# Performance work log

Hardware: AMD Instinct MI355X
Metric: run time of the kernel (lower is better)

## Reference

```python
import jax, jax.numpy as jnp
import numpy as np

DIM = 256; N_HEADS = 8; HEAD_DIM = DIM // N_HEADS
RELU_DIM = 1024; LN_DIM = 512; N_LN = 2; EMB_DIM = 256
VOCAB = 32000; N_CLASSES = 16; B = 8; SEQ = 256
N_ITERS = 12   # fixed-point iterations of the DEQ solve (ITFn2)
EPS = 1e-5     # torch LayerNorm default eps


def sinusoidal_pos_emb(T, d):
    pos = np.arange(T)[:, None].astype(np.float32)
    i = np.arange(d // 2)[None, :].astype(np.float32)
    ang = pos / np.power(10000.0, 2.0 * i / d)
    pe = np.zeros((T, d), np.float32)
    pe[:, 0::2] = np.sin(ang)
    pe[:, 1::2] = np.cos(ang)
    return jnp.asarray(pe)


def setup_inputs() -> dict:
    key = jax.random.key(0)
    ks = jax.random.split(key, 8)
    x = jax.random.randint(ks[0], (B, SEQ), 0, VOCAB)
    seq_lens = jax.random.randint(ks[1], (B,), 1, SEQ + 1)
    emb = jax.random.normal(ks[2], (VOCAB + 1, EMB_DIM), jnp.float32) * EMB_DIM ** -0.5
    emb = emb.at[VOCAB].set(0.0)  # padding_idx row
    cls_token = jax.random.normal(ks[3], (1, 1, EMB_DIM), jnp.float32) * EMB_DIM ** -0.5
    # scaled down vs kaiming so the fixed-point map is contractive (module enforces this via project())
    A = jax.random.normal(ks[4], (RELU_DIM + LN_DIM, RELU_DIM + LN_DIM + DIM + EMB_DIM), jnp.float32) * 0.01
    b = jnp.zeros((RELU_DIM + LN_DIM,), jnp.float32)
    A_qkv = jax.random.normal(ks[5], (3 * DIM, LN_DIM), jnp.float32) * (2.0 / LN_DIM) ** 0.5
    W_cls = jax.random.normal(ks[6], (N_CLASSES, RELU_DIM + LN_DIM + DIM), jnp.float32) * (RELU_DIM + LN_DIM + DIM) ** -0.5
    b_cls = jnp.zeros((N_CLASSES,), jnp.float32)
    return {"x": x, "seq_lens": seq_lens, "emb": emb, "cls_token": cls_token,
            "A": A, "A_qkv": A_qkv, "b": b, "W_cls": W_cls, "b_cls": b_cls}


def reference(x, seq_lens, emb, cls_token, A, A_qkv, b, W_cls, b_cls):
    Bsz, T = x.shape
    Tp = T + 1
    # input injection: embed + sinusoidal pos, then prepend cls token
    u = emb[x] + sinusoidal_pos_emb(T, EMB_DIM)[None]
    u = jnp.concatenate([jnp.broadcast_to(cls_token, (Bsz, 1, EMB_DIM)), u], axis=1)  # (B, T+1, E)
    pos = jnp.arange(Tp)
    src_mask = (seq_lens[:, None] + 1) <= pos[None]  # (B, T+1), True = padded key
    # A_qkv rows ordered (n_heads, 3, head_dim) per scale_by_S rearrange
    Wqkv = A_qkv.reshape(N_HEADS, 3, HEAD_DIM, LN_DIM)
    scale = 1.0 / jnp.sqrt(jnp.asarray(HEAD_DIM, u.dtype))
    neg = jnp.asarray(-1e9, u.dtype)

    def step(z, _):
        # pre-activations for relu + layernorm blocks
        pre = jnp.einsum('btj,ij->bti', jnp.concatenate([z, u], axis=-1), A) + b
        z_r = jax.nn.relu(pre[..., :RELU_DIM])
        zl = pre[..., RELU_DIM:].reshape(Bsz, Tp, N_LN, LN_DIM // N_LN)
        mu = zl.mean(-1, keepdims=True)
        var = zl.var(-1, keepdims=True)
        z_l = ((zl - mu) * jax.lax.rsqrt(var + EPS)).reshape(Bsz, Tp, LN_DIM)
        # multi-head attention driven by the layernorm block
        qkv = jnp.einsum('btj,hmdj->bthmd', z_l, Wqkv)  # (B, T+1, H, 3, hd)
        q, k, v = qkv[..., 0, :], qkv[..., 1, :], qkv[..., 2, :]
        scores = jnp.einsum('bqhd,bkhd->bhqk', q, k) * scale
        scores = jnp.where(src_mask[:, None, None, :], neg, scores)
        attn = jax.nn.softmax(scores, axis=-1)
        z_a = jnp.einsum('bhqk,bkhd->bqhd', attn, v).reshape(Bsz, Tp, DIM)
        return jnp.concatenate([z_r, z_l, z_a], axis=-1), None

    z0 = jnp.zeros((Bsz, Tp, RELU_DIM + LN_DIM + DIM), u.dtype)
    z, _ = jax.lax.scan(step, z0, None, length=N_ITERS)
    # classify from the equilibrium cls-token state
    return z[:, 0] @ W_cls.T + b_cls
```

## Files before the change

### kernel.cpp

```cpp
#include <hip/hip_runtime.h>
#include <hip/hip_bf16.h>
#include <math.h>

#define TP 257
#define ROWS 2056
#define XDIM 2048
#define ZDIM 1792
#define PREDIM 1536
#define QKVDIM 768
#define EMBD 256

using f32x4  = __attribute__((ext_vector_type(4))) float;
using bf16x8 = __attribute__((ext_vector_type(8))) short;

__device__ __forceinline__ ushort f2bf(float f) {
    uint32_t u = __float_as_uint(f);
    return (ushort)((u + 0x7fffu + ((u >> 16) & 1u)) >> 16);
}
__device__ __forceinline__ float bf2f(ushort u) {
    return __uint_as_float(((uint32_t)u) << 16);
}

#define GLD16(g, l) __builtin_amdgcn_global_load_lds( \
    (const __attribute__((address_space(1))) void*)(g), \
    (__attribute__((address_space(3))) void*)(l), 16, 0, 0)

__global__ __launch_bounds__(256) void f2bf_kernel(
    const float* __restrict__ in, ushort* __restrict__ out, int n)
{
    int i = blockIdx.x * 256 + threadIdx.x;
    if (i < n) out[i] = f2bf(in[i]);
}

__global__ __launch_bounds__(256) void build_u_kernel(
    const int* __restrict__ x, const float* __restrict__ emb,
    const float* __restrict__ cls, ushort* __restrict__ xbA, ushort* __restrict__ xbB)
{
    int row = blockIdx.x;
    int e   = threadIdx.x;
    int b = row / TP, t = row % TP;
    float val;
    if (t == 0) {
        val = cls[e];
    } else {
        int tt = t - 1;
        int xi = x[b * 256 + tt];
        float ang = (float)tt * expf(-(float)(e & ~1) * 0.035978672652993f);
        float pe  = (e & 1) ? cosf(ang) : sinf(ang);
        val = emb[(size_t)xi * EMBD + e] + pe;
    }
    ushort bv = f2bf(val);
    xbA[(size_t)row * XDIM + 1792 + e] = bv;
    xbB[(size_t)row * XDIM + 1792 + e] = bv;
}

__global__ __launch_bounds__(256) void gemm_bf16_kernel(
    const ushort* __restrict__ X, int ldx,
    const ushort* __restrict__ W,
    const float* __restrict__ bias,
    float* __restrict__ C, ushort* __restrict__ Cb,
    int ldc, int M, int N, int Ksplit, int Ktotal, size_t splitStride)
{
    __shared__ ushort As[128 * 32];
    __shared__ ushort Bs[128 * 32];
    int tid  = threadIdx.x;
    int lane = tid & 63, wv = tid >> 6;
    int wr = wv >> 1, wc = wv & 1;
    int r0 = blockIdx.x * 128, c0 = blockIdx.y * 128;
    int kbeg = blockIdx.z * Ksplit;
    int kfin = kbeg + Ksplit;

    f32x4 acc[4][4] = {};

    int srow = wv * 32 + (lane >> 2);
    int skol = (lane & 3) * 8;
    int fk   = (lane >> 4) * 8;

    for (int k0 = kbeg; k0 < kfin; k0 += 32) {
        #pragma unroll
        for (int i = 0; i < 2; ++i) {
            int rr = r0 + srow + i * 16;
            if (rr >= M) rr = M - 1;
            const ushort* ga = X + (size_t)rr * ldx + k0 + skol;
            GLD16(ga, &As[(wv * 32 + i * 16) * 32]);
            const ushort* gb = W + (size_t)(c0 + srow + i * 16) * Ktotal + k0 + skol;
            GLD16(gb, &Bs[(wv * 32 + i * 16) * 32]);
        }
        __syncthreads();

        bf16x8 a[4], b[4];
        #pragma unroll
        for (int m = 0; m < 4; ++m)
            a[m] = *(const bf16x8*)&As[(wr * 64 + m * 16 + (lane & 15)) * 32 + fk];
        #pragma unroll
        for (int n = 0; n < 4; ++n)
            b[n] = *(const bf16x8*)&Bs[(wc * 64 + n * 16 + (lane & 15)) * 32 + fk];
        #pragma unroll
        for (int m = 0; m < 4; ++m)
            #pragma unroll
            for (int n = 0; n < 4; ++n)
                acc[m][n] = __builtin_amdgcn_mfma_f32_16x16x32_bf16(a[m], b[n], acc[m][n], 0, 0, 0);
        __syncthreads();
    }

    int crow = (lane >> 4) * 4;
    int ccol = lane & 15;
    float* Cz = C ? C + (size_t)blockIdx.z * splitStride : nullptr;
    bool addb = (bias != nullptr) && (blockIdx.z == 0);
    #pragma unroll
    for (int m = 0; m < 4; ++m) {
        #pragma unroll
        for (int j = 0; j < 4; ++j) {
            int r = r0 + wr * 64 + m * 16 + crow + j;
            if (r < M) {
                #pragma unroll
                for (int n = 0; n < 4; ++n) {
                    int cc = n * 16 + ccol;
                    float vb = addb ? bias[c0 + wc * 64 + cc] : 0.0f;
                    float v = acc[m][n][j] + vb;
                    if (Cb) Cb[(size_t)r * ldc + c0 + wc * 64 + cc] = f2bf(v);
                    else    Cz[(size_t)r * ldc + c0 + wc * 64 + cc] = v;
                }
            }
        }
    }
}

__global__ __launch_bounds__(256) void relu_ln_kernel(
    const float* __restrict__ pre0, const float* __restrict__ pre1,
    ushort* __restrict__ zb)
{
    int row = blockIdx.x;
    int tid = threadIdx.x;
    const float* p0 = pre0 + (size_t)row * PREDIM;
    const float* p1 = pre1 ? pre1 + (size_t)row * PREDIM : nullptr;
    ushort* zr = zb + (size_t)row * XDIM;

    float4 v = *(const float4*)(p0 + 4 * tid);
    if (p1) {
        float4 w = *(const float4*)(p1 + 4 * tid);
        v.x += w.x; v.y += w.y; v.z += w.z; v.w += w.w;
    }
    ushort4 o;
    o.x = f2bf(v.x > 0.f ? v.x : 0.f);
    o.y = f2bf(v.y > 0.f ? v.y : 0.f);
    o.z = f2bf(v.z > 0.f ? v.z : 0.f);
    o.w = f2bf(v.w > 0.f ? v.w : 0.f);
    *(ushort4*)(zr + 4 * tid) = o;

    __shared__ float warr[4][2];
    #pragma unroll
    for (int g = 0; g < 2; ++g) {
        int c = 1024 + g * 256 + tid;
        float xv = p0[c] + (p1 ? p1[c] : 0.f);
        float s = xv, s2 = xv * xv;
        #pragma unroll
        for (int off = 32; off; off >>= 1) {
            s  += __shfl_down(s, off);
            s2 += __shfl_down(s2, off);
        }
        int wave = tid >> 6, lane = tid & 63;
        if (lane == 0) { warr[wave][0] = s; warr[wave][1] = s2; }
        __syncthreads();
        float ts  = warr[0][0] + warr[1][0] + warr[2][0] + warr[3][0];
        float ts2 = warr[0][1] + warr[1][1] + warr[2][1] + warr[3][1];
        float mu  = ts * (1.0f / 256.0f);
        float var = ts2 * (1.0f / 256.0f) - mu * mu;
        float y = (xv - mu) * rsqrtf(var + 1e-5f);
        zr[c] = f2bf(y);
        __syncthreads();
    }
}

__global__ __launch_bounds__(256) void attn_kernel(
    const ushort* __restrict__ qkvb, const int* __restrict__ seq_lens,
    ushort* __restrict__ zb)
{
    __shared__ ushort Kl[288 * 40];
    __shared__ ushort VTl[32 * 296];
    __shared__ ushort Pl[4][16 * 40];

    int bh = blockIdx.x;
    int b = bh >> 3, h = bh & 7;
    int kend = seq_lens[b] + 1; if (kend > TP) kend = TP;
    int tid = threadIdx.x;
    const size_t qbase = (size_t)(b * TP) * QKVDIM + h * 96;

    for (int idx = tid; idx < 31 * 32; idx += 256) {
        int row = 257 + (idx >> 5), d = idx & 31;
        Kl[row * 40 + d] = 0;
    }
    for (int idx = tid; idx < 32 * 32; idx += 256) {
        int d = idx >> 5, col = 257 + (idx & 31);
        VTl[d * 296 + col] = 0;
    }
    for (int idx = tid; idx < 257 * 4; idx += 256) {
        int row = idx >> 2, seg = idx & 3;
        *(bf16x8*)&Kl[row * 40 + seg * 8] =
            *(const bf16x8*)&qkvb[qbase + (size_t)row * QKVDIM + 32 + seg * 8];
    }
    for (int idx = tid; idx < 257 * 32; idx += 256) {
        int key = idx >> 5, d = idx & 31;
        VTl[d * 296 + key] = qkvb[qbase + (size_t)key * QKVDIM + 64 + d];
    }
    __syncthreads();

    int wave = tid >> 6, lane = tid & 63;
    int q0 = blockIdx.y * 64 + wave * 16;
    if (q0 > 256) return;
    int qcol = lane & 15, g = lane >> 4;
    int ktmax = (kend + 15) >> 4;
    const float scale = 0.17677669529663687f;

    int qg = q0 + qcol; if (qg > 256) qg = 256;
    bf16x8 aq = *(const bf16x8*)&qkvb[qbase + (size_t)qg * QKVDIM + g * 8];

    f32x4 s[17];
    const f32x4 zz = {};
    #pragma unroll
    for (int kt = 0; kt < 17; ++kt) {
        s[kt] = (f32x4)(-1e30f);
        if (kt < ktmax) {
            bf16x8 bk = *(const bf16x8*)&Kl[(kt * 16 + qcol) * 40 + g * 8];
            f32x4 r = __builtin_amdgcn_mfma_f32_16x16x32_bf16(aq, bk, zz, 0, 0, 0);
            bool kv = (kt * 16 + qcol) < kend;
            #pragma unroll
            for (int j = 0; j < 4; ++j)
                s[kt][j] = kv ? r[j] * scale : -1e30f;
        }
    }

    float m0[4], l0[4];
    #pragma unroll
    for (int j = 0; j < 4; ++j) m0[j] = -3.0e38f;
    #pragma unroll
    for (int kt = 0; kt < 17; ++kt)
        #pragma unroll
        for (int j = 0; j < 4; ++j) m0[j] = fmaxf(m0[j], s[kt][j]);
    #pragma unroll
    for (int j = 0; j < 4; ++j) {
        #pragma unroll
        for (int off = 1; off < 16; off <<= 1)
            m0[j] = fmaxf(m0[j], __shfl_xor(m0[j], off));
        l0[j] = 0.f;
    }
    #pragma unroll
    for (int kt = 0; kt < 17; ++kt)
        #pragma unroll
        for (int j = 0; j < 4; ++j) {
            float p = __expf(s[kt][j] - m0[j]);
            s[kt][j] = p;
            l0[j] += p;
        }
    #pragma unroll
    for (int j = 0; j < 4; ++j) {
        #pragma unroll
        for (int off = 1; off < 16; off <<= 1)
            l0[j] += __shfl_xor(l0[j], off);
        l0[j] = 1.0f / l0[j];
    }
    #pragma unroll
    for (int kt = 0; kt < 17; ++kt)
        #pragma unroll
        for (int j = 0; j < 4; ++j) s[kt][j] *= l0[j];

    f32x4 o[2] = {};
    ushort* Pw = Pl[wave];
    #pragma unroll
    for (int c = 0; c < 9; ++c) {
        if (c * 32 < kend) {
            #pragma unroll
            for (int t = 0; t < 2; ++t)
                #pragma unroll
                for (int j = 0; j < 4; ++j)
                    Pw[(g * 4 + j) * 40 + t * 16 + qcol] = f2bf(s[2 * c + t][j]);
            bf16x8 pa = *(const bf16x8*)&Pw[qcol * 40 + g * 8];
            #pragma unroll
            for (int n = 0; n < 2; ++n) {
                bf16x8 vb = *(const bf16x8*)&VTl[(n * 16 + qcol) * 296 + c * 32 + g * 8];
                o[n] = __builtin_amdgcn_mfma_f32_16x16x32_bf16(pa, vb, o[n], 0, 0, 0);
            }
        }
    }

    #pragma unroll
    for (int n = 0; n < 2; ++n)
        #pragma unroll
        for (int j = 0; j < 4; ++j) {
            int q = q0 + g * 4 + j;
            if (q <= 256)
                zb[(size_t)(b * TP + q) * XDIM + PREDIM + h * 32 + n * 16 + qcol] =
                    f2bf(o[n][j]);
        }
}

__global__ __launch_bounds__(64) void cls_kernel(
    const ushort* __restrict__ zb, const float* __restrict__ W,
    const float* __restrict__ bias, float* __restrict__ out)
{
    int o = blockIdx.x;
    int c = o & 15, b = o >> 4;
    int lane = threadIdx.x;
    const ushort* zr = zb + (size_t)(b * TP) * XDIM;
    const float* wr = W + (size_t)c * ZDIM;
    float s = 0.f;
    for (int j = lane; j < ZDIM; j += 64) s += bf2f(zr[j]) * wr[j];
    #pragma unroll
    for (int off = 32; off; off >>= 1) s += __shfl_down(s, off);
    if (lane == 0) out[b * 16 + c] = s + bias[c];
}

extern "C" void kernel_launch(void* const* d_in, const int* in_sizes, int n_in,
                              void* d_out, int out_size, void* d_ws, size_t ws_size,
                              hipStream_t stream) {
    const int*   x        = (const int*)d_in[0];
    const int*   seq_lens = (const int*)d_in[1];
    const float* emb      = (const float*)d_in[2];
    const float* cls      = (const float*)d_in[3];
    const float* A        = (const float*)d_in[4];
    const float* A_qkv    = (const float*)d_in[5];
    const float* b        = (const float*)d_in[6];
    const float* W_cls    = (const float*)d_in[7];
    const float* b_cls    = (const float*)d_in[8];
    float* out = (float*)d_out;

    ushort* XbA  = (ushort*)d_ws;
    ushort* XbB  = XbA + (size_t)ROWS * XDIM;
    ushort* Ab   = XbB + (size_t)ROWS * XDIM;
    ushort* Aqb  = Ab + (size_t)PREDIM * 2048;
    float*  pre0 = (float*)(Aqb + (size_t)QKVDIM * 512);
    float*  pre1 = pre0 + (size_t)ROWS * PREDIM;
    ushort* qkvb = (ushort*)pre0;

    size_t need2 = (size_t)((char*)(pre1 + (size_t)ROWS * PREDIM) - (char*)d_ws);
    int nsplit = (ws_size >= need2) ? 2 : 1;

    hipMemsetAsync(XbA, 0, (size_t)ROWS * XDIM * sizeof(ushort), stream);
    f2bf_kernel<<<(PREDIM * 2048 + 255) / 256, 256, 0, stream>>>(A, Ab, PREDIM * 2048);
    f2bf_kernel<<<(QKVDIM * 512 + 255) / 256, 256, 0, stream>>>(A_qkv, Aqb, QKVDIM * 512);
    build_u_kernel<<<ROWS, 256, 0, stream>>>(x, emb, cls, XbA, XbB);

    ushort* cur = XbA;
    ushort* nxt = XbB;
    for (int it = 0; it < 12; ++it) {
        gemm_bf16_kernel<<<dim3(17, 12, nsplit), 256, 0, stream>>>(
            cur, XDIM, Ab, b, pre0, nullptr, PREDIM, ROWS, PREDIM,
            2048 / nsplit, 2048, (size_t)ROWS * PREDIM);
        relu_ln_kernel<<<ROWS, 256, 0, stream>>>(
            pre0, nsplit == 2 ? pre1 : nullptr, nxt);
        gemm_bf16_kernel<<<dim3(17, 6, 1), 256, 0, stream>>>(
            nxt + 1024, XDIM, Aqb, nullptr, nullptr, qkvb, QKVDIM, ROWS, QKVDIM,
            512, 512, 0);
        attn_kernel<<<dim3(64, 5), 256, 0, stream>>>(qkvb, seq_lens, nxt);
        ushort* tmp = cur; cur = nxt; nxt = tmp;
    }
    cls_kernel<<<128, 64, 0, stream>>>(cur, W_cls, b_cls, out);
}
```

Before: 1.014 ms.

## Double-buffer GEMM LDS tiles and raise split-K to four

The GEMM now uses two LDS buffers per operand and issues the global-to-LDS loads for the next K tile before computing on the current one, with one barrier per step. This lets memory latency overlap with MFMA work. The main pre-activation GEMM also splits K four ways when the workspace is large enough, so 17x12x4 blocks fill more of the CUs. The relu/LN kernel is generalised to sum any number of partial buffers. The cost is extra partial-sum traffic (4x fp32 pre buffers read back each iteration) and double the LDS per block, which may lower occupancy.

Result: slower. 1.053 ms (+3.9%).

```diff
diff --git a/kernel.cpp b/kernel.cpp
--- a/kernel.cpp
+++ b/kernel.cpp
@@ -61,8 +61,8 @@
     float* __restrict__ C, ushort* __restrict__ Cb,
     int ldc, int M, int N, int Ksplit, int Ktotal, size_t splitStride)
 {
-    __shared__ ushort As[128 * 32];
-    __shared__ ushort Bs[128 * 32];
+    __shared__ ushort As[2][128 * 32];
+    __shared__ ushort Bs[2][128 * 32];
     int tid  = threadIdx.x;
     int lane = tid & 63, wv = tid >> 6;
     int wr = wv >> 1, wc = wv & 1;
@@ -76,31 +76,40 @@
     int skol = (lane & 3) * 8;
     int fk   = (lane >> 4) * 8;
 
-    for (int k0 = kbeg; k0 < kfin; k0 += 32) {
+    auto stage = [&](int buf, int k0) {
         #pragma unroll
         for (int i = 0; i < 2; ++i) {
             int rr = r0 + srow + i * 16;
             if (rr >= M) rr = M - 1;
             const ushort* ga = X + (size_t)rr * ldx + k0 + skol;
-            GLD16(ga, &As[(wv * 32 + i * 16) * 32]);
+            GLD16(ga, &As[buf][(wv * 32 + i * 16) * 32]);
             const ushort* gb = W + (size_t)(c0 + srow + i * 16) * Ktotal + k0 + skol;
-            GLD16(gb, &Bs[(wv * 32 + i * 16) * 32]);
-        }
-        __syncthreads();
+            GLD16(gb, &Bs[buf][(wv * 32 + i * 16) * 32]);
+        }
+    };
+
+    stage(0, kbeg);
+    __syncthreads();
+    int cur = 0;
+
+    for (int k0 = kbeg; k0 < kfin; k0 += 32) {
+        if (k0 + 32 < kfin) stage(cur ^ 1, k0 + 32);
 
         bf16x8 a[4], b[4];
         #pragma unroll
         for (int m = 0; m < 4; ++m)
-            a[m] = *(const bf16x8*)&As[(wr * 64 + m * 16 + (lane & 15)) * 32 + fk];
+            a[m] = *(const bf16x8*)&As[cur][(wr * 64 + m * 16 + (lane & 15)) * 32 + fk];
         #pragma unroll
         for (int n = 0; n < 4; ++n)
-            b[n] = *(const bf16x8*)&Bs[(wc * 64 + n * 16 + (lane & 15)) * 32 + fk];
+            b[n] = *(const bf16x8*)&Bs[cur][(wc * 64 + n * 16 + (lane & 15)) * 32 + fk];
         #pragma unroll
         for (int m = 0; m < 4; ++m)
             #pragma unroll
             for (int n = 0; n < 4; ++n)
                 acc[m][n] = __builtin_amdgcn_mfma_f32_16x16x32_bf16(a[m], b[n], acc[m][n], 0, 0, 0);
+
         __syncthreads();
+        cur ^= 1;
     }
 
     int crow = (lane >> 4) * 4;
@@ -127,18 +136,17 @@
 }
 
 __global__ __launch_bounds__(256) void relu_ln_kernel(
-    const float* __restrict__ pre0, const float* __restrict__ pre1,
+    const float* __restrict__ pre, int nsplit, size_t splitStride,
     ushort* __restrict__ zb)
 {
     int row = blockIdx.x;
     int tid = threadIdx.x;
-    const float* p0 = pre0 + (size_t)row * PREDIM;
-    const float* p1 = pre1 ? pre1 + (size_t)row * PREDIM : nullptr;
+    const float* p0 = pre + (size_t)row * PREDIM;
     ushort* zr = zb + (size_t)row * XDIM;
 
     float4 v = *(const float4*)(p0 + 4 * tid);
-    if (p1) {
-        float4 w = *(const float4*)(p1 + 4 * tid);
+    for (int s = 1; s < nsplit; ++s) {
+        float4 w = *(const float4*)(p0 + s * splitStride + 4 * tid);
         v.x += w.x; v.y += w.y; v.z += w.z; v.w += w.w;
     }
     ushort4 o;
@@ -152,7 +160,8 @@
     #pragma unroll
     for (int g = 0; g < 2; ++g) {
         int c = 1024 + g * 256 + tid;
-        float xv = p0[c] + (p1 ? p1[c] : 0.f);
+        float xv = p0[c];
+        for (int s = 1; s < nsplit; ++s) xv += p0[s * splitStride + c];
         float s = xv, s2 = xv * xv;
         #pragma unroll
         for (int off = 32; off; off >>= 1) {
@@ -328,12 +337,14 @@
     ushort* XbB  = XbA + (size_t)ROWS * XDIM;
     ushort* Ab   = XbB + (size_t)ROWS * XDIM;
     ushort* Aqb  = Ab + (size_t)PREDIM * 2048;
-    float*  pre0 = (float*)(Aqb + (size_t)QKVDIM * 512);
-    float*  pre1 = pre0 + (size_t)ROWS * PREDIM;
-    ushort* qkvb = (ushort*)pre0;
-
-    size_t need2 = (size_t)((char*)(pre1 + (size_t)ROWS * PREDIM) - (char*)d_ws);
-    int nsplit = (ws_size >= need2) ? 2 : 1;
+    float*  pre  = (float*)(Aqb + (size_t)QKVDIM * 512);
+    ushort* qkvb = (ushort*)pre;
+
+    const size_t sstride = (size_t)ROWS * PREDIM;
+    size_t base = (size_t)((char*)pre - (char*)d_ws);
+    int nsplit = 1;
+    if (ws_size >= base + 4 * sstride * sizeof(float)) nsplit = 4;
+    else if (ws_size >= base + 2 * sstride * sizeof(float)) nsplit = 2;
 
     hipMemsetAsync(XbA, 0, (size_t)ROWS * XDIM * sizeof(ushort), stream);
     f2bf_kernel<<<(PREDIM * 2048 + 255) / 256, 256, 0, stream>>>(A, Ab, PREDIM * 2048);
@@ -344,10 +355,9 @@
     ushort* nxt = XbB;
     for (int it = 0; it < 12; ++it) {
         gemm_bf16_kernel<<<dim3(17, 12, nsplit), 256, 0, stream>>>(
-            cur, XDIM, Ab, b, pre0, nullptr, PREDIM, ROWS, PREDIM,
-            2048 / nsplit, 2048, (size_t)ROWS * PREDIM);
-        relu_ln_kernel<<<ROWS, 256, 0, stream>>>(
-            pre0, nsplit == 2 ? pre1 : nullptr, nxt);
+            cur, XDIM, Ab, b, pre, nullptr, PREDIM, ROWS, PREDIM,
+            2048 / nsplit, 2048, sstride);
+        relu_ln_kernel<<<ROWS, 256, 0, stream>>>(pre, nsplit, sstride, nxt);
         gemm_bf16_kernel<<<dim3(17, 6, 1), 256, 0, stream>>>(
             nxt + 1024, XDIM, Aqb, nullptr, nullptr, qkvb, QKVDIM, ROWS, QKVDIM,
             512, 512, 0);
```
